# Kernel tuning notes

Measured on AMD Instinct MI355X. Metric: run time of the kernel, lower is better.

Reference implementation:

```python
import jax, jax.numpy as jnp
import numpy as np

B, T, C = 8, 512, 1024
H, E = 16, 64          # n_head, head_dim; H*E == C
L = 2048               # cached (prefix) length in the KV cache


def setup_inputs() -> dict:
    key = jax.random.key(0)
    ks = jax.random.split(key, 6)
    scale = 0.02
    return {
        "x": jax.random.normal(ks[0], (B, T, C), jnp.float32),
        "k_cache": jax.random.normal(ks[1], (B, H, L, E), jnp.float32),
        "v_cache": jax.random.normal(ks[2], (B, H, L, E), jnp.float32),
        "Wqkv": jax.random.normal(ks[3], (C, 3 * C), jnp.float32) * scale,
        "bqkv": jnp.zeros((3 * C,), jnp.float32),
        "Wproj": jax.random.normal(ks[4], (C, C), jnp.float32) * scale,
        "bproj": jnp.zeros((C,), jnp.float32),
    }


def reference(x, k_cache, v_cache, Wqkv, bqkv, Wproj, bproj):
    qkv = x @ Wqkv + bqkv
    q, k, v = jnp.split(qkv, 3, axis=-1)

    def to_heads(t):
        return t.reshape(B, T, H, E).transpose(0, 2, 1, 3)

    q, k, v = to_heads(q), to_heads(k), to_heads(v)

    # append new k,v to the cache (kv_cache.update + get)
    k_full = jnp.concatenate([k_cache, k], axis=2)  # (B,H,L+T,E)
    v_full = jnp.concatenate([v_cache, v], axis=2)

    # manual self-attention with cache-offset causal mask: row i (global pos L+i)
    # may attend to cols j <= L+i  (bias[L:L+T, :L+T])
    att = jnp.einsum("bhte,bhse->bhts", q, k_full) * (1.0 / np.sqrt(E))
    i = jnp.arange(T)[:, None] + L
    j = jnp.arange(L + T)[None, :]
    att = jnp.where(j <= i, att, -jnp.inf)
    att = jax.nn.softmax(att, axis=-1)

    y = jnp.einsum("bhts,bhse->bhte", att, v_full)
    y = y.transpose(0, 2, 1, 3).reshape(B, T, C)
    return y @ Wproj + bproj
```

## Files before the change

### kernel.cpp

```cpp
#include <hip/hip_runtime.h>
#include <hip/hip_bf16.h>

typedef unsigned short u16;
typedef unsigned int u32;

constexpr int B_ = 8, T_ = 512, C_ = 1024, H_ = 16, E_ = 64, L_ = 2048;
constexpr int S_ = L_ + T_;

typedef __bf16 bf16x8 __attribute__((ext_vector_type(8)));
typedef float f32x4 __attribute__((ext_vector_type(4)));
typedef float f32x16 __attribute__((ext_vector_type(16)));

#define QSCALE 0.18033688011112042f

__device__ inline u16 f2bf(float f) {
  u32 u = __float_as_uint(f);
  u32 r = (u + 0x7fffu + ((u >> 16) & 1u)) >> 16;
  return (u16)r;
}

__device__ inline u32 pk2(float a, float b) {
  union { __hip_bfloat162 h; u32 u; } cv;
  cv.h = __float22bfloat162_rn(float2{a, b});
  return cv.u;
}

__device__ inline void pl32swap(u32& a, u32& b) {
  asm("v_permlane32_swap_b32 %0, %1" : "+v"(a), "+v"(b));
}

__device__ inline void gload_lds16(const u16* g, u16* l) {
  __builtin_amdgcn_global_load_lds(
      (const __attribute__((address_space(1))) u32*)g,
      (__attribute__((address_space(3))) u32*)l, 16, 0, 0);
}

__global__ __launch_bounds__(256) void convert_f32_bf16(const float* __restrict__ in,
                                                        u16* __restrict__ out) {
  const int i = blockIdx.x * 256 + threadIdx.x;
  const float4 a0 = ((const float4*)in)[i * 2];
  const float4 a1 = ((const float4*)in)[i * 2 + 1];
  uint4 p;
  p.x = pk2(a0.x, a0.y);
  p.y = pk2(a0.z, a0.w);
  p.z = pk2(a1.x, a1.y);
  p.w = pk2(a1.z, a1.w);
  ((uint4*)out)[i] = p;
}

__global__ __launch_bounds__(256) void transpose_f32_bf16(const float* __restrict__ in,
                                                          u16* __restrict__ out,
                                                          int R, int Ccols) {
  __shared__ u16 tile[64][65];
  const int r0 = blockIdx.y * 64;
  const int c0 = blockIdx.x * 64;
  const int tr = threadIdx.x >> 6;
  const int tc = threadIdx.x & 63;
#pragma unroll
  for (int i = 0; i < 16; ++i)
    tile[tr + i * 4][tc] = f2bf(in[(size_t)(r0 + tr + i * 4) * Ccols + c0 + tc]);
  __syncthreads();
#pragma unroll
  for (int i = 0; i < 16; ++i)
    out[(size_t)(c0 + tr + i * 4) * R + r0 + tc] = tile[tc][tr + i * 4];
}

__global__ __launch_bounds__(256) void prep_kv(const float* __restrict__ kc,
                                               const float* __restrict__ vc,
                                               u16* __restrict__ Km,
                                               u16* __restrict__ Vtm) {
  __shared__ u16 vt[64 * 72];
  const int s0 = (blockIdx.x & 31) * 64;
  const int bh = blockIdx.x >> 5;
  const int tid = threadIdx.x;
  const int srow = tid >> 2;
  const int eq = (tid & 3) * 16;

  {
    const float* kp = kc + ((size_t)bh * L_ + s0 + srow) * E_ + eq;
    float kv[16];
    *(float4*)(kv + 0) = *(const float4*)(kp + 0);
    *(float4*)(kv + 4) = *(const float4*)(kp + 4);
    *(float4*)(kv + 8) = *(const float4*)(kp + 8);
    *(float4*)(kv + 12) = *(const float4*)(kp + 12);
    uint4 p0, p1;
    p0.x = pk2(kv[0], kv[1]);
    p0.y = pk2(kv[2], kv[3]);
    p0.z = pk2(kv[4], kv[5]);
    p0.w = pk2(kv[6], kv[7]);
    p1.x = pk2(kv[8], kv[9]);
    p1.y = pk2(kv[10], kv[11]);
    p1.z = pk2(kv[12], kv[13]);
    p1.w = pk2(kv[14], kv[15]);
    u16* kd = Km + ((size_t)bh * S_ + s0 + srow) * E_ + eq;
    *(uint4*)kd = p0;
    *(uint4*)(kd + 8) = p1;
  }
  {
    const float* vp = vc + ((size_t)bh * L_ + s0 + srow) * E_ + eq;
    float vv[16];
    *(float4*)(vv + 0) = *(const float4*)(vp + 0);
    *(float4*)(vv + 4) = *(const float4*)(vp + 4);
    *(float4*)(vv + 8) = *(const float4*)(vp + 8);
    *(float4*)(vv + 12) = *(const float4*)(vp + 12);
    uint4 p0, p1;
    p0.x = pk2(vv[0], vv[1]);
    p0.y = pk2(vv[2], vv[3]);
    p0.z = pk2(vv[4], vv[5]);
    p0.w = pk2(vv[6], vv[7]);
    p1.x = pk2(vv[8], vv[9]);
    p1.y = pk2(vv[10], vv[11]);
    p1.z = pk2(vv[12], vv[13]);
    p1.w = pk2(vv[14], vv[15]);
    *(uint4*)(vt + srow * 72 + eq) = p0;
    *(uint4*)(vt + srow * 72 + eq + 8) = p1;
  }
  __syncthreads();
  {
    const int erow = tid >> 2;
    const int sq = (tid & 3) * 16;
    u16 o[16];
#pragma unroll
    for (int j = 0; j < 16; ++j) o[j] = vt[(sq + j) * 72 + erow];
    u16* vd = Vtm + ((size_t)bh * E_ + erow) * S_ + s0 + sq;
    *(uint4*)vd = *(uint4*)(o + 0);
    *(uint4*)(vd + 8) = *(uint4*)(o + 8);
  }
}

template <int MODE>
__global__ __launch_bounds__(256) void gemm128(const u16* __restrict__ A,
                                               const u16* __restrict__ BT,
                                               const float* __restrict__ bias,
                                               u16* __restrict__ qh,
                                               u16* __restrict__ Km,
                                               u16* __restrict__ Vtm,
                                               float* __restrict__ outf,
                                               int M, int N, int K) {
  __shared__ __align__(16) u16 As[128 * 32];
  __shared__ __align__(16) u16 Bs[128 * 32];
  const int tid = threadIdx.x;
  const int lane = tid & 63;
  const int w = tid >> 6;
  const int m0 = blockIdx.y * 128;
  const int n0 = blockIdx.x * 128;
  const int wm = (w >> 1) * 64;
  const int wn = (w & 1) * 64;
  const int fm = lane & 15;
  const int fk = (lane >> 4) * 8;

  const int srow = w * 16 + (lane >> 2);
  const int scol = (lane & 3) * 8;
  const u16* Ag = A + (size_t)(m0 + srow) * K + scol;
  const u16* Bg = BT + (size_t)(n0 + srow) * K + scol;
  u16* AsU = As + w * 512;
  u16* BsU = Bs + w * 512;

  f32x4 acc[4][4];
#pragma unroll
  for (int i = 0; i < 4; ++i)
#pragma unroll
    for (int j = 0; j < 4; ++j) acc[i][j] = f32x4{0.f, 0.f, 0.f, 0.f};

  for (int k0 = 0; k0 < K; k0 += 32) {
    gload_lds16(Ag, AsU);
    gload_lds16(Ag + (size_t)64 * K, AsU + 2048);
    gload_lds16(Bg, BsU);
    gload_lds16(Bg + (size_t)64 * K, BsU + 2048);
    Ag += 32;
    Bg += 32;
    __syncthreads();
    bf16x8 af[4], bf[4];
#pragma unroll
    for (int i = 0; i < 4; ++i)
      af[i] = *(const bf16x8*)(As + (wm + i * 16 + fm) * 32 + fk);
#pragma unroll
    for (int j = 0; j < 4; ++j)
      bf[j] = *(const bf16x8*)(Bs + (wn + j * 16 + fm) * 32 + fk);
#pragma unroll
    for (int i = 0; i < 4; ++i)
#pragma unroll
      for (int j = 0; j < 4; ++j)
        acc[i][j] = __builtin_amdgcn_mfma_f32_16x16x32_bf16(af[i], bf[j], acc[i][j], 0, 0, 0);
    __syncthreads();
  }

  const int rbase = (lane >> 4) * 4;
  const int cbase = lane & 15;
#pragma unroll
  for (int i = 0; i < 4; ++i)
#pragma unroll
    for (int j = 0; j < 4; ++j) {
      const int n = n0 + wn + j * 16 + cbase;
      const float bv = bias[n];
#pragma unroll
      for (int r = 0; r < 4; ++r) {
        const int m = m0 + wm + i * 16 + rbase + r;
        const float v = acc[i][j][r] + bv;
        if (MODE == 0) {
          const int seg = n >> 10;
          const int c = n & 1023;
          const int e = c & 63;
          const int bhh = ((m >> 9) * H_) + (c >> 6);
          const int t = m & 511;
          if (seg == 0)
            qh[((size_t)bhh * T_ + t) * E_ + e] = f2bf(v * QSCALE);
          else if (seg == 1)
            Km[((size_t)bhh * S_ + L_ + t) * E_ + e] = f2bf(v);
          else
            Vtm[((size_t)bhh * E_ + e) * S_ + L_ + t] = f2bf(v);
        } else {
          outf[(size_t)m * N + n] = v;
        }
      }
    }
}

__global__ __launch_bounds__(256, 2) void attn_v4(const u16* __restrict__ qh,
                                                  const u16* __restrict__ Km,
                                                  const u16* __restrict__ Vtm,
                                                  u16* __restrict__ y2) {
  __shared__ __align__(16) u16 Ks[2][64 * 64];
  __shared__ __align__(16) u16 Vts[2][64 * 64];

  const int tid = threadIdx.x;
  const int lane = tid & 63;
  const int w = tid >> 6;
  const int bh = blockIdx.x & 127;
  const int qt = blockIdx.x >> 7;
  const int h = bh & (H_ - 1);
  const int b = bh >> 4;
  const int t0 = qt * 128;

  const int ln = lane & 31;
  const int hi = lane >> 5;
  const int swz = ln & 7;

  const u16* qbase = qh + ((size_t)bh * T_ + t0 + w * 32 + ln) * E_;
  bf16x8 qf[4];
#pragma unroll
  for (int et = 0; et < 4; ++et)
    qf[et] = *(const bf16x8*)(qbase + et * 16 + hi * 8);

  const int srow = tid >> 2;
  const int su = (tid & 3) * 2;
  const u16* kg = Km + ((size_t)bh * S_ + srow) * E_ + su * 8;
  const u16* vg = Vtm + ((size_t)bh * E_ + srow) * S_ + su * 8;
  const int st0 = srow * 64 + ((su ^ (srow & 7)) * 8);
  const int st1 = srow * 64 + (((su + 1) ^ (srow & 7)) * 8);

  f32x16 Yt[2], lacc;
#pragma unroll
  for (int i = 0; i < 16; ++i) {
    Yt[0][i] = 0.f;
    Yt[1][i] = 0.f;
    lacc[i] = 0.f;
  }

  const bf16x8 ones = {(__bf16)1.f, (__bf16)1.f, (__bf16)1.f, (__bf16)1.f,
                       (__bf16)1.f, (__bf16)1.f, (__bf16)1.f, (__bf16)1.f};

  const int qmin_w = L_ + t0 + w * 32;
  const int nchunk = (L_ + t0 + 128) >> 6;

  uint4 kr0 = *(const uint4*)(kg);
  uint4 kr1 = *(const uint4*)(kg + 8);
  uint4 vr0 = *(const uint4*)(vg);
  uint4 vr1 = *(const uint4*)(vg + 8);
  {
    u16* kd = Ks[0];
    u16* vd = Vts[0];
    *(uint4*)(kd + st0) = kr0;
    *(uint4*)(kd + st1) = kr1;
    *(uint4*)(vd + st0) = vr0;
    *(uint4*)(vd + st1) = vr1;
  }
  __syncthreads();

  for (int c = 0; c < nchunk; ++c) {
    const int sbase = c << 6;
    const u16* ks = Ks[c & 1];
    const u16* vs = Vts[c & 1];
    const bool more = (c + 1 < nchunk);

    if (more) {
      const size_t ko = (size_t)(c + 1) * 64 * E_;
      const int vo = (c + 1) * 64;
      kr0 = *(const uint4*)(kg + ko);
      kr1 = *(const uint4*)(kg + ko + 8);
      vr0 = *(const uint4*)(vg + vo);
      vr1 = *(const uint4*)(vg + vo + 8);
    }

    if (sbase <= qmin_w + 31) {
      bf16x8 pa[4];
#pragma unroll
      for (int kb = 0; kb < 2; ++kb) {
        f32x16 s;
#pragma unroll
        for (int i = 0; i < 16; ++i) s[i] = 0.f;
#pragma unroll
        for (int et = 0; et < 4; ++et) {
          const bf16x8 kf = *(const bf16x8*)(
              ks + (kb * 32 + ln) * 64 + (((et * 2 + hi) ^ swz) * 8));
          s = __builtin_amdgcn_mfma_f32_32x32x16_bf16(kf, qf[et], s, 0, 0, 0);
        }

        if (sbase + 63 > qmin_w) {
          const int qpos = qmin_w + ln;
          const int kb0 = sbase + kb * 32 + hi * 4;
#pragma unroll
          for (int r = 0; r < 16; ++r) {
            const int keypos = kb0 + (r & 3) + 8 * (r >> 2);
            if (keypos > qpos) s[r] = -1e30f;
          }
        }

#pragma unroll
        for (int r = 0; r < 16; ++r) s[r] = exp2f(s[r]);

#pragma unroll
        for (int t = 0; t < 2; ++t) {
          u32 x0 = pk2(s[8 * t + 0], s[8 * t + 1]);
          u32 y0 = pk2(s[8 * t + 4], s[8 * t + 5]);
          u32 x1 = pk2(s[8 * t + 2], s[8 * t + 3]);
          u32 y1 = pk2(s[8 * t + 6], s[8 * t + 7]);
          pl32swap(x0, y0);
          pl32swap(x1, y1);
          union { u32 u[4]; bf16x8 v; } pu;
          pu.u[0] = x0;
          pu.u[1] = x1;
          pu.u[2] = y0;
          pu.u[3] = y1;
          pa[kb * 2 + t] = pu.v;
        }
      }

#pragma unroll
      for (int t = 0; t < 4; ++t)
        lacc = __builtin_amdgcn_mfma_f32_32x32x16_bf16(ones, pa[t], lacc, 0, 0, 0);

#pragma unroll
      for (int eb = 0; eb < 2; ++eb)
#pragma unroll
        for (int t = 0; t < 4; ++t) {
          const bf16x8 vf = *(const bf16x8*)(
              vs + (eb * 32 + ln) * 64 + (((t * 2 + hi) ^ swz) * 8));
          Yt[eb] = __builtin_amdgcn_mfma_f32_32x32x16_bf16(vf, pa[t], Yt[eb], 0, 0, 0);
        }
    }

    if (more) {
      u16* kd = Ks[(c + 1) & 1];
      u16* vd = Vts[(c + 1) & 1];
      *(uint4*)(kd + st0) = kr0;
      *(uint4*)(kd + st1) = kr1;
      *(uint4*)(vd + st0) = vr0;
      *(uint4*)(vd + st1) = vr1;
    }
    __syncthreads();
  }

  const float rl = 1.f / lacc[0];
  const int t_out = t0 + w * 32 + ln;
  u16* yp = y2 + ((size_t)b * T_ + t_out) * C_ + h * E_ + hi * 4;
#pragma unroll
  for (int eb = 0; eb < 2; ++eb)
#pragma unroll
    for (int g = 0; g < 4; ++g) {
      uint2 st;
      st.x = pk2(Yt[eb][4 * g + 0] * rl, Yt[eb][4 * g + 1] * rl);
      st.y = pk2(Yt[eb][4 * g + 2] * rl, Yt[eb][4 * g + 3] * rl);
      *(uint2*)(yp + eb * 32 + g * 8) = st;
    }
}

extern "C" void kernel_launch(void* const* d_in, const int* in_sizes, int n_in,
                              void* d_out, int out_size, void* d_ws, size_t ws_size,
                              hipStream_t stream) {
  const float* x = (const float*)d_in[0];
  const float* kc = (const float*)d_in[1];
  const float* vc = (const float*)d_in[2];
  const float* Wqkv = (const float*)d_in[3];
  const float* bqkv = (const float*)d_in[4];
  const float* Wproj = (const float*)d_in[5];
  const float* bproj = (const float*)d_in[6];
  float* out = (float*)d_out;

  u16* qh = (u16*)d_ws;
  u16* y2 = qh + 4194304;
  u16* xb = y2 + 4194304;
  u16* WqT = xb + 4194304;
  u16* WpT = WqT + 3145728;
  u16* Km = WpT + 1048576;
  u16* Vtm = Km + 20971520;

  convert_f32_bf16<<<dim3(2048), 256, 0, stream>>>(x, xb);
  transpose_f32_bf16<<<dim3(48, 16), 256, 0, stream>>>(Wqkv, WqT, 1024, 3072);
  transpose_f32_bf16<<<dim3(16, 16), 256, 0, stream>>>(Wproj, WpT, 1024, 1024);
  prep_kv<<<dim3(128 * 32), 256, 0, stream>>>(kc, vc, Km, Vtm);

  gemm128<0><<<dim3(24, 32), 256, 0, stream>>>(xb, WqT, bqkv, qh, Km, Vtm, nullptr,
                                               4096, 3072, 1024);

  attn_v4<<<dim3(512), 256, 0, stream>>>(qh, Km, Vtm, y2);

  gemm128<1><<<dim3(8, 32), 256, 0, stream>>>(y2, WpT, bproj, nullptr, nullptr,
                                              nullptr, out, 4096, 1024, 1024);
}
```

Baseline: 343.6 us.

## Load K/V fragments directly from global in attention; stage new V via transpose kernel

The attention kernel stops staging K and V tiles through double-buffered shared memory with block barriers. Each wave now loads its K and V MFMA fragments straight from global memory and software-pipelines the next K chunk in registers. Each wave also computes its own causal chunk count and applies the mask only on its last chunk. The QKV GEMM now writes new V rows coalesced into a scratch buffer (y2), and a separate vtrans kernel transposes them into the V-transposed cache, avoiding strided scatter stores. The cost is extra global and L2 traffic with no cross-wave reuse of K/V through LDS, one more kernel launch, and higher register pressure.

Result: slower. 408.1 us (+18.8%).

```diff
diff --git a/kernel.cpp b/kernel.cpp
--- a/kernel.cpp
+++ b/kernel.cpp
@@ -128,13 +128,35 @@
   }
 }
 
+__global__ __launch_bounds__(256) void vtrans(const u16* __restrict__ vh,
+                                              u16* __restrict__ Vtm) {
+  __shared__ u16 vt[64 * 72];
+  const int t0 = (blockIdx.x & 7) * 64;
+  const int bh = blockIdx.x >> 3;
+  const int tid = threadIdx.x;
+  const int srow = tid >> 2;
+  const int eq = (tid & 3) * 16;
+  const u16* vp = vh + ((size_t)bh * T_ + t0 + srow) * E_ + eq;
+  *(uint4*)(vt + srow * 72 + eq) = *(const uint4*)vp;
+  *(uint4*)(vt + srow * 72 + eq + 8) = *(const uint4*)(vp + 8);
+  __syncthreads();
+  const int erow = tid >> 2;
+  const int sq = (tid & 3) * 16;
+  u16 o[16];
+#pragma unroll
+  for (int j = 0; j < 16; ++j) o[j] = vt[(sq + j) * 72 + erow];
+  u16* vd = Vtm + ((size_t)bh * E_ + erow) * S_ + L_ + t0 + sq;
+  *(uint4*)vd = *(uint4*)(o + 0);
+  *(uint4*)(vd + 8) = *(uint4*)(o + 8);
+}
+
 template <int MODE>
 __global__ __launch_bounds__(256) void gemm128(const u16* __restrict__ A,
                                                const u16* __restrict__ BT,
                                                const float* __restrict__ bias,
                                                u16* __restrict__ qh,
                                                u16* __restrict__ Km,
-                                               u16* __restrict__ Vtm,
+                                               u16* __restrict__ vout,
                                                float* __restrict__ outf,
                                                int M, int N, int K) {
   __shared__ __align__(16) u16 As[128 * 32];
@@ -208,7 +230,7 @@
           else if (seg == 1)
             Km[((size_t)bhh * S_ + L_ + t) * E_ + e] = f2bf(v);
           else
-            Vtm[((size_t)bhh * E_ + e) * S_ + L_ + t] = f2bf(v);
+            vout[((size_t)bhh * T_ + t) * E_ + e] = f2bf(v);
         } else {
           outf[(size_t)m * N + n] = v;
         }
@@ -216,13 +238,58 @@
     }
 }
 
-__global__ __launch_bounds__(256, 2) void attn_v4(const u16* __restrict__ qh,
+#define ATTN_CHUNK(KF, KN, cc)                                                   \
+  {                                                                              \
+    const int sbase = (cc) << 6;                                                 \
+    const int cpf = ((cc) + 1 < nck) ? (cc) + 1 : nck - 1;                       \
+    bf16x8 vf[2][4];                                                             \
+    _Pragma("unroll") for (int eb = 0; eb < 2; ++eb)                             \
+      _Pragma("unroll") for (int t = 0; t < 4; ++t)                              \
+        vf[eb][t] = *(const bf16x8*)(Vl + (size_t)eb * 32 * S_ + (cc) * 64 + t * 16); \
+    bf16x8 pa[4];                                                                \
+    _Pragma("unroll") for (int kb = 0; kb < 2; ++kb) {                           \
+      f32x16 s;                                                                  \
+      _Pragma("unroll") for (int i = 0; i < 16; ++i) s[i] = 0.f;                 \
+      _Pragma("unroll") for (int et = 0; et < 4; ++et)                           \
+        s = __builtin_amdgcn_mfma_f32_32x32x16_bf16(KF[kb][et], qf[et], s, 0, 0, 0); \
+      if ((cc) == nck - 1) {                                                     \
+        const int mb = sbase + kb * 32 + hi * 4;                                 \
+        _Pragma("unroll") for (int r = 0; r < 16; ++r) {                         \
+          const int keypos = mb + (r & 3) + 8 * (r >> 2);                        \
+          if (keypos > qpos) s[r] = -1e30f;                                      \
+        }                                                                        \
+      }                                                                          \
+      _Pragma("unroll") for (int r = 0; r < 16; ++r) s[r] = exp2f(s[r]);         \
+      _Pragma("unroll") for (int t = 0; t < 2; ++t) {                            \
+        u32 x0 = pk2(s[8 * t + 0], s[8 * t + 1]);                                \
+        u32 y0 = pk2(s[8 * t + 4], s[8 * t + 5]);                                \
+        u32 x1 = pk2(s[8 * t + 2], s[8 * t + 3]);                                \
+        u32 y1 = pk2(s[8 * t + 6], s[8 * t + 7]);                                \
+        pl32swap(x0, y0);                                                        \
+        pl32swap(x1, y1);                                                        \
+        union { u32 u[4]; bf16x8 v; } pu;                                        \
+        pu.u[0] = x0;                                                            \
+        pu.u[1] = x1;                                                            \
+        pu.u[2] = y0;                                                            \
+        pu.u[3] = y1;                                                            \
+        pa[kb * 2 + t] = pu.v;                                                   \
+      }                                                                          \
+    }                                                                            \
+    _Pragma("unroll") for (int kb = 0; kb < 2; ++kb)                             \
+      _Pragma("unroll") for (int et = 0; et < 4; ++et)                           \
+        KN[kb][et] = *(const bf16x8*)(Kl + ((size_t)cpf * 64 + kb * 32) * E_ + et * 16); \
+    _Pragma("unroll") for (int t = 0; t < 4; ++t)                                \
+      lacc = __builtin_amdgcn_mfma_f32_32x32x16_bf16(ones, pa[t], lacc, 0, 0, 0); \
+    _Pragma("unroll") for (int t = 0; t < 4; ++t)                                \
+      Yt[0] = __builtin_amdgcn_mfma_f32_32x32x16_bf16(vf[0][t], pa[t], Yt[0], 0, 0, 0); \
+    _Pragma("unroll") for (int t = 0; t < 4; ++t)                                \
+      Yt[1] = __builtin_amdgcn_mfma_f32_32x32x16_bf16(vf[1][t], pa[t], Yt[1], 0, 0, 0); \
+  }
+
+__global__ __launch_bounds__(256, 2) void attn_v5(const u16* __restrict__ qh,
                                                   const u16* __restrict__ Km,
                                                   const u16* __restrict__ Vtm,
                                                   u16* __restrict__ y2) {
-  __shared__ __align__(16) u16 Ks[2][64 * 64];
-  __shared__ __align__(16) u16 Vts[2][64 * 64];
-
   const int tid = threadIdx.x;
   const int lane = tid & 63;
   const int w = tid >> 6;
@@ -234,7 +301,6 @@
 
   const int ln = lane & 31;
   const int hi = lane >> 5;
-  const int swz = ln & 7;
 
   const u16* qbase = qh + ((size_t)bh * T_ + t0 + w * 32 + ln) * E_;
   bf16x8 qf[4];
@@ -242,12 +308,12 @@
   for (int et = 0; et < 4; ++et)
     qf[et] = *(const bf16x8*)(qbase + et * 16 + hi * 8);
 
-  const int srow = tid >> 2;
-  const int su = (tid & 3) * 2;
-  const u16* kg = Km + ((size_t)bh * S_ + srow) * E_ + su * 8;
-  const u16* vg = Vtm + ((size_t)bh * E_ + srow) * S_ + su * 8;
-  const int st0 = srow * 64 + ((su ^ (srow & 7)) * 8);
-  const int st1 = srow * 64 + (((su + 1) ^ (srow & 7)) * 8);
+  const int qmin = L_ + t0 + w * 32;
+  const int qpos = qmin + ln;
+  const int nck = (qmin + 32 + 63) >> 6;
+
+  const u16* Kl = Km + ((size_t)bh * S_ + ln) * E_ + hi * 8;
+  const u16* Vl = Vtm + ((size_t)bh * E_ + ln) * S_ + hi * 8;
 
   f32x16 Yt[2], lacc;
 #pragma unroll
@@ -260,105 +326,19 @@
   const bf16x8 ones = {(__bf16)1.f, (__bf16)1.f, (__bf16)1.f, (__bf16)1.f,
                        (__bf16)1.f, (__bf16)1.f, (__bf16)1.f, (__bf16)1.f};
 
-  const int qmin_w = L_ + t0 + w * 32;
-  const int nchunk = (L_ + t0 + 128) >> 6;
-
-  uint4 kr0 = *(const uint4*)(kg);
-  uint4 kr1 = *(const uint4*)(kg + 8);
-  uint4 vr0 = *(const uint4*)(vg);
-  uint4 vr1 = *(const uint4*)(vg + 8);
-  {
-    u16* kd = Ks[0];
-    u16* vd = Vts[0];
-    *(uint4*)(kd + st0) = kr0;
-    *(uint4*)(kd + st1) = kr1;
-    *(uint4*)(vd + st0) = vr0;
-    *(uint4*)(vd + st1) = vr1;
-  }
-  __syncthreads();
-
-  for (int c = 0; c < nchunk; ++c) {
-    const int sbase = c << 6;
-    const u16* ks = Ks[c & 1];
-    const u16* vs = Vts[c & 1];
-    const bool more = (c + 1 < nchunk);
-
-    if (more) {
-      const size_t ko = (size_t)(c + 1) * 64 * E_;
-      const int vo = (c + 1) * 64;
-      kr0 = *(const uint4*)(kg + ko);
-      kr1 = *(const uint4*)(kg + ko + 8);
-      vr0 = *(const uint4*)(vg + vo);
-      vr1 = *(const uint4*)(vg + vo + 8);
-    }
-
-    if (sbase <= qmin_w + 31) {
-      bf16x8 pa[4];
-#pragma unroll
-      for (int kb = 0; kb < 2; ++kb) {
-        f32x16 s;
-#pragma unroll
-        for (int i = 0; i < 16; ++i) s[i] = 0.f;
-#pragma unroll
-        for (int et = 0; et < 4; ++et) {
-          const bf16x8 kf = *(const bf16x8*)(
-              ks + (kb * 32 + ln) * 64 + (((et * 2 + hi) ^ swz) * 8));
-          s = __builtin_amdgcn_mfma_f32_32x32x16_bf16(kf, qf[et], s, 0, 0, 0);
-        }
-
-        if (sbase + 63 > qmin_w) {
-          const int qpos = qmin_w + ln;
-          const int kb0 = sbase + kb * 32 + hi * 4;
-#pragma unroll
-          for (int r = 0; r < 16; ++r) {
-            const int keypos = kb0 + (r & 3) + 8 * (r >> 2);
-            if (keypos > qpos) s[r] = -1e30f;
-          }
-        }
-
-#pragma unroll
-        for (int r = 0; r < 16; ++r) s[r] = exp2f(s[r]);
-
-#pragma unroll
-        for (int t = 0; t < 2; ++t) {
-          u32 x0 = pk2(s[8 * t + 0], s[8 * t + 1]);
-          u32 y0 = pk2(s[8 * t + 4], s[8 * t + 5]);
-          u32 x1 = pk2(s[8 * t + 2], s[8 * t + 3]);
-          u32 y1 = pk2(s[8 * t + 6], s[8 * t + 7]);
-          pl32swap(x0, y0);
-          pl32swap(x1, y1);
-          union { u32 u[4]; bf16x8 v; } pu;
-          pu.u[0] = x0;
-          pu.u[1] = x1;
-          pu.u[2] = y0;
-          pu.u[3] = y1;
-          pa[kb * 2 + t] = pu.v;
-        }
-      }
-
-#pragma unroll
-      for (int t = 0; t < 4; ++t)
-        lacc = __builtin_amdgcn_mfma_f32_32x32x16_bf16(ones, pa[t], lacc, 0, 0, 0);
-
-#pragma unroll
-      for (int eb = 0; eb < 2; ++eb)
-#pragma unroll
-        for (int t = 0; t < 4; ++t) {
-          const bf16x8 vf = *(const bf16x8*)(
-              vs + (eb * 32 + ln) * 64 + (((t * 2 + hi) ^ swz) * 8));
-          Yt[eb] = __builtin_amdgcn_mfma_f32_32x32x16_bf16(vf, pa[t], Yt[eb], 0, 0, 0);
-        }
-    }
-
-    if (more) {
-      u16* kd = Ks[(c + 1) & 1];
-      u16* vd = Vts[(c + 1) & 1];
-      *(uint4*)(kd + st0) = kr0;
-      *(uint4*)(kd + st1) = kr1;
-      *(uint4*)(vd + st0) = vr0;
-      *(uint4*)(vd + st1) = vr1;
-    }
-    __syncthreads();
+  bf16x8 kA[2][4], kB[2][4];
+#pragma unroll
+  for (int kb = 0; kb < 2; ++kb)
+#pragma unroll
+    for (int et = 0; et < 4; ++et)
+      kA[kb][et] = *(const bf16x8*)(Kl + (size_t)(kb * 32) * E_ + et * 16);
+
+  int c = 0;
+  while (true) {
+    ATTN_CHUNK(kA, kB, c);
+    if (++c >= nck) break;
+    ATTN_CHUNK(kB, kA, c);
+    if (++c >= nck) break;
   }
 
   const float rl = 1.f / lacc[0];
@@ -400,10 +380,11 @@
   transpose_f32_bf16<<<dim3(16, 16), 256, 0, stream>>>(Wproj, WpT, 1024, 1024);
   prep_kv<<<dim3(128 * 32), 256, 0, stream>>>(kc, vc, Km, Vtm);
 
-  gemm128<0><<<dim3(24, 32), 256, 0, stream>>>(xb, WqT, bqkv, qh, Km, Vtm, nullptr,
+  gemm128<0><<<dim3(24, 32), 256, 0, stream>>>(xb, WqT, bqkv, qh, Km, y2, nullptr,
                                                4096, 3072, 1024);
-
-  attn_v4<<<dim3(512), 256, 0, stream>>>(qh, Km, Vtm, y2);
+  vtrans<<<dim3(128 * 8), 256, 0, stream>>>(y2, Vtm);
+
+  attn_v5<<<dim3(512), 256, 0, stream>>>(qh, Km, Vtm, y2);
 
   gemm128<1><<<dim3(8, 32), 256, 0, stream>>>(y2, WpT, bproj, nullptr, nullptr,
                                               nullptr, out, 4096, 1024, 1024);
```

## Split KV chunks across two wave groups in attention and coalesce V transpose

Applied to the files above, without the earlier changes.

The attention kernel now runs 512 threads per block. Two groups of four waves each process alternate 64-key chunks for the same 128 queries, and their partial outputs and row sums are merged through shared memory at the end. The QKV GEMM now writes new V values row-major into a scratch buffer, and a separate vtrans kernel transposes them into the V-transposed cache, replacing the scattered strided stores. The goal is more parallelism and latency hiding per block and better store coalescing. The cost is an extra kernel launch, a larger shared-memory footprint, and a reduction step at the end.

Result: slower. 355.4 us (+3.4%).

```diff
diff --git a/kernel.cpp b/kernel.cpp
--- a/kernel.cpp
+++ b/kernel.cpp
@@ -128,13 +128,35 @@
   }
 }
 
+__global__ __launch_bounds__(256) void vtrans(const u16* __restrict__ vh,
+                                              u16* __restrict__ Vtm) {
+  __shared__ u16 vt[64 * 72];
+  const int t0 = (blockIdx.x & 7) * 64;
+  const int bh = blockIdx.x >> 3;
+  const int tid = threadIdx.x;
+  const int srow = tid >> 2;
+  const int eq = (tid & 3) * 16;
+  const u16* vp = vh + ((size_t)bh * T_ + t0 + srow) * E_ + eq;
+  *(uint4*)(vt + srow * 72 + eq) = *(const uint4*)vp;
+  *(uint4*)(vt + srow * 72 + eq + 8) = *(const uint4*)(vp + 8);
+  __syncthreads();
+  const int erow = tid >> 2;
+  const int sq = (tid & 3) * 16;
+  u16 o[16];
+#pragma unroll
+  for (int j = 0; j < 16; ++j) o[j] = vt[(sq + j) * 72 + erow];
+  u16* vd = Vtm + ((size_t)bh * E_ + erow) * S_ + L_ + t0 + sq;
+  *(uint4*)vd = *(uint4*)(o + 0);
+  *(uint4*)(vd + 8) = *(uint4*)(o + 8);
+}
+
 template <int MODE>
 __global__ __launch_bounds__(256) void gemm128(const u16* __restrict__ A,
                                                const u16* __restrict__ BT,
                                                const float* __restrict__ bias,
                                                u16* __restrict__ qh,
                                                u16* __restrict__ Km,
-                                               u16* __restrict__ Vtm,
+                                               u16* __restrict__ vout,
                                                float* __restrict__ outf,
                                                int M, int N, int K) {
   __shared__ __align__(16) u16 As[128 * 32];
@@ -208,7 +230,7 @@
           else if (seg == 1)
             Km[((size_t)bhh * S_ + L_ + t) * E_ + e] = f2bf(v);
           else
-            Vtm[((size_t)bhh * E_ + e) * S_ + L_ + t] = f2bf(v);
+            vout[((size_t)bhh * T_ + t) * E_ + e] = f2bf(v);
         } else {
           outf[(size_t)m * N + n] = v;
         }
@@ -216,16 +238,19 @@
     }
 }
 
-__global__ __launch_bounds__(256, 2) void attn_v4(const u16* __restrict__ qh,
+__global__ __launch_bounds__(512, 4) void attn_v6(const u16* __restrict__ qh,
                                                   const u16* __restrict__ Km,
                                                   const u16* __restrict__ Vtm,
                                                   u16* __restrict__ y2) {
-  __shared__ __align__(16) u16 Ks[2][64 * 64];
-  __shared__ __align__(16) u16 Vts[2][64 * 64];
+  __shared__ __align__(16) u16 smem[32768];
+  u16* KsB = smem;
+  u16* VtsB = smem + 16384;
 
   const int tid = threadIdx.x;
   const int lane = tid & 63;
   const int w = tid >> 6;
+  const int wq = w & 3;
+  const int par = w >> 2;
   const int bh = blockIdx.x & 127;
   const int qt = blockIdx.x >> 7;
   const int h = bh & (H_ - 1);
@@ -236,40 +261,47 @@
   const int hi = lane >> 5;
   const int swz = ln & 7;
 
-  const u16* qbase = qh + ((size_t)bh * T_ + t0 + w * 32 + ln) * E_;
+  const u16* qbase = qh + ((size_t)bh * T_ + t0 + wq * 32 + ln) * E_;
   bf16x8 qf[4];
 #pragma unroll
   for (int et = 0; et < 4; ++et)
     qf[et] = *(const bf16x8*)(qbase + et * 16 + hi * 8);
 
-  const int srow = tid >> 2;
-  const int su = (tid & 3) * 2;
+  const int tq = tid & 255;
+  const int sp = tid >> 8;
+  const int srow = tq >> 2;
+  const int su = (tq & 3) * 2;
   const u16* kg = Km + ((size_t)bh * S_ + srow) * E_ + su * 8;
   const u16* vg = Vtm + ((size_t)bh * E_ + srow) * S_ + su * 8;
   const int st0 = srow * 64 + ((su ^ (srow & 7)) * 8);
   const int st1 = srow * 64 + (((su + 1) ^ (srow & 7)) * 8);
 
-  f32x16 Yt[2], lacc;
+  f32x16 Yt[2], lacc, zero16;
 #pragma unroll
   for (int i = 0; i < 16; ++i) {
     Yt[0][i] = 0.f;
     Yt[1][i] = 0.f;
     lacc[i] = 0.f;
+    zero16[i] = 0.f;
   }
 
   const bf16x8 ones = {(__bf16)1.f, (__bf16)1.f, (__bf16)1.f, (__bf16)1.f,
                        (__bf16)1.f, (__bf16)1.f, (__bf16)1.f, (__bf16)1.f};
 
-  const int qmin_w = L_ + t0 + w * 32;
+  const int qmin_w = L_ + t0 + wq * 32;
+  const int qpos = qmin_w + ln;
   const int nchunk = (L_ + t0 + 128) >> 6;
-
-  uint4 kr0 = *(const uint4*)(kg);
-  uint4 kr1 = *(const uint4*)(kg + 8);
-  uint4 vr0 = *(const uint4*)(vg);
-  uint4 vr1 = *(const uint4*)(vg + 8);
+  const int npair = nchunk >> 1;
+
   {
-    u16* kd = Ks[0];
-    u16* vd = Vts[0];
+    const size_t ko = (size_t)sp * 64 * E_;
+    const int vo = sp * 64;
+    uint4 kr0 = *(const uint4*)(kg + ko);
+    uint4 kr1 = *(const uint4*)(kg + ko + 8);
+    uint4 vr0 = *(const uint4*)(vg + vo);
+    uint4 vr1 = *(const uint4*)(vg + vo + 8);
+    u16* kd = KsB + sp * 4096;
+    u16* vd = VtsB + sp * 4096;
     *(uint4*)(kd + st0) = kr0;
     *(uint4*)(kd + st1) = kr1;
     *(uint4*)(vd + st0) = vr0;
@@ -277,41 +309,42 @@
   }
   __syncthreads();
 
-  for (int c = 0; c < nchunk; ++c) {
-    const int sbase = c << 6;
-    const u16* ks = Ks[c & 1];
-    const u16* vs = Vts[c & 1];
-    const bool more = (c + 1 < nchunk);
-
+  for (int i = 0; i < npair; ++i) {
+    const int hlf = i & 1;
+    const int cs = 2 * (i + 1) + sp;
+    const bool more = cs < nchunk;
+    uint4 kr0, kr1, vr0, vr1;
     if (more) {
-      const size_t ko = (size_t)(c + 1) * 64 * E_;
-      const int vo = (c + 1) * 64;
+      const size_t ko = (size_t)cs * 64 * E_;
+      const int vo = cs * 64;
       kr0 = *(const uint4*)(kg + ko);
       kr1 = *(const uint4*)(kg + ko + 8);
       vr0 = *(const uint4*)(vg + vo);
       vr1 = *(const uint4*)(vg + vo + 8);
     }
 
+    const int cmy = 2 * i + par;
+    const int sbase = cmy << 6;
     if (sbase <= qmin_w + 31) {
+      const u16* ks = KsB + (hlf * 2 + par) * 4096;
+      const u16* vs = VtsB + (hlf * 2 + par) * 4096;
       bf16x8 pa[4];
 #pragma unroll
       for (int kb = 0; kb < 2; ++kb) {
         f32x16 s;
-#pragma unroll
-        for (int i = 0; i < 16; ++i) s[i] = 0.f;
 #pragma unroll
         for (int et = 0; et < 4; ++et) {
           const bf16x8 kf = *(const bf16x8*)(
               ks + (kb * 32 + ln) * 64 + (((et * 2 + hi) ^ swz) * 8));
-          s = __builtin_amdgcn_mfma_f32_32x32x16_bf16(kf, qf[et], s, 0, 0, 0);
+          s = __builtin_amdgcn_mfma_f32_32x32x16_bf16(kf, qf[et],
+                                                      et == 0 ? zero16 : s, 0, 0, 0);
         }
 
         if (sbase + 63 > qmin_w) {
-          const int qpos = qmin_w + ln;
-          const int kb0 = sbase + kb * 32 + hi * 4;
+          const int mb = sbase + kb * 32 + hi * 4;
 #pragma unroll
           for (int r = 0; r < 16; ++r) {
-            const int keypos = kb0 + (r & 3) + 8 * (r >> 2);
+            const int keypos = mb + (r & 3) + 8 * (r >> 2);
             if (keypos > qpos) s[r] = -1e30f;
           }
         }
@@ -351,8 +384,8 @@
     }
 
     if (more) {
-      u16* kd = Ks[(c + 1) & 1];
-      u16* vd = Vts[(c + 1) & 1];
+      u16* kd = KsB + ((hlf ^ 1) * 2 + sp) * 4096;
+      u16* vd = VtsB + ((hlf ^ 1) * 2 + sp) * 4096;
       *(uint4*)(kd + st0) = kr0;
       *(uint4*)(kd + st1) = kr1;
       *(uint4*)(vd + st0) = vr0;
@@ -361,18 +394,36 @@
     __syncthreads();
   }
 
-  const float rl = 1.f / lacc[0];
-  const int t_out = t0 + w * 32 + ln;
-  u16* yp = y2 + ((size_t)b * T_ + t_out) * C_ + h * E_ + hi * 4;
-#pragma unroll
-  for (int eb = 0; eb < 2; ++eb)
-#pragma unroll
-    for (int g = 0; g < 4; ++g) {
-      uint2 st;
-      st.x = pk2(Yt[eb][4 * g + 0] * rl, Yt[eb][4 * g + 1] * rl);
-      st.y = pk2(Yt[eb][4 * g + 2] * rl, Yt[eb][4 * g + 3] * rl);
-      *(uint2*)(yp + eb * 32 + g * 8) = st;
-    }
+  float* red = (float*)smem;
+  if (par == 1) {
+    float* rp = red + ((size_t)(wq * 64 + lane)) * 34;
+#pragma unroll
+    for (int i = 0; i < 16; ++i) rp[i] = Yt[0][i];
+#pragma unroll
+    for (int i = 0; i < 16; ++i) rp[16 + i] = Yt[1][i];
+    rp[32] = lacc[0];
+  }
+  __syncthreads();
+  if (par == 0) {
+    const float* rp = red + ((size_t)(wq * 64 + lane)) * 34;
+#pragma unroll
+    for (int i = 0; i < 16; ++i) Yt[0][i] += rp[i];
+#pragma unroll
+    for (int i = 0; i < 16; ++i) Yt[1][i] += rp[16 + i];
+    const float rl = 1.f / (lacc[0] + rp[32]);
+
+    const int t_out = t0 + wq * 32 + ln;
+    u16* yp = y2 + ((size_t)b * T_ + t_out) * C_ + h * E_ + hi * 4;
+#pragma unroll
+    for (int eb = 0; eb < 2; ++eb)
+#pragma unroll
+      for (int g = 0; g < 4; ++g) {
+        uint2 st;
+        st.x = pk2(Yt[eb][4 * g + 0] * rl, Yt[eb][4 * g + 1] * rl);
+        st.y = pk2(Yt[eb][4 * g + 2] * rl, Yt[eb][4 * g + 3] * rl);
+        *(uint2*)(yp + eb * 32 + g * 8) = st;
+      }
+  }
 }
 
 extern "C" void kernel_launch(void* const* d_in, const int* in_sizes, int n_in,
@@ -400,10 +451,11 @@
   transpose_f32_bf16<<<dim3(16, 16), 256, 0, stream>>>(Wproj, WpT, 1024, 1024);
   prep_kv<<<dim3(128 * 32), 256, 0, stream>>>(kc, vc, Km, Vtm);
 
-  gemm128<0><<<dim3(24, 32), 256, 0, stream>>>(xb, WqT, bqkv, qh, Km, Vtm, nullptr,
+  gemm128<0><<<dim3(24, 32), 256, 0, stream>>>(xb, WqT, bqkv, qh, Km, y2, nullptr,
                                                4096, 3072, 1024);
-
-  attn_v4<<<dim3(512), 256, 0, stream>>>(qh, Km, Vtm, y2);
+  vtrans<<<dim3(128 * 8), 256, 0, stream>>>(y2, Vtm);
+
+  attn_v6<<<dim3(512), 512, 0, stream>>>(qh, Km, Vtm, y2);
 
   gemm128<1><<<dim3(8, 32), 256, 0, stream>>>(y2, WpT, bproj, nullptr, nullptr,
                                               nullptr, out, 4096, 1024, 1024);
```

## Pre-swizzle K/V in global memory and stream tiles via direct global-to-LDS loads

Applied to the files above, without the earlier changes.

The attention kernel stops staging K/V tiles through registers. It now issues global_load_lds transfers straight into a triple-buffered LDS ring, prefetching two chunks ahead and synchronising with explicit vmcnt waits and barriers. Because the direct-to-LDS path cannot apply the XOR swizzle, the producers (prep_kv and the QKV GEMM epilogue) now write K and V^T into global memory already swizzled. pk2 also switches to an inline v_cvt_pk_bf16_f32 instruction, and the first MFMA of each score tile now starts from a zero accumulator. This trades a larger LDS footprint and tighter coupling of layouts across kernels for less register pressure and more overlap of memory traffic with compute.

Measured after the change: 335.7 us. 2.3% less time.

```diff
diff --git a/kernel.cpp b/kernel.cpp
--- a/kernel.cpp
+++ b/kernel.cpp
@@ -12,6 +12,7 @@
 typedef float f32x16 __attribute__((ext_vector_type(16)));
 
 #define QSCALE 0.18033688011112042f
+
 
 __device__ inline u16 f2bf(float f) {
   u32 u = __float_as_uint(f);
@@ -20,9 +21,9 @@
 }
 
 __device__ inline u32 pk2(float a, float b) {
-  union { __hip_bfloat162 h; u32 u; } cv;
-  cv.h = __float22bfloat162_rn(float2{a, b});
-  return cv.u;
+  u32 r;
+  asm("v_cvt_pk_bf16_f32 %0, %1, %2" : "=v"(r) : "v"(a), "v"(b));
+  return r;
 }
 
 __device__ inline void pl32swap(u32& a, u32& b) {
@@ -92,9 +93,10 @@
     p1.y = pk2(kv[10], kv[11]);
     p1.z = pk2(kv[12], kv[13]);
     p1.w = pk2(kv[14], kv[15]);
-    u16* kd = Km + ((size_t)bh * S_ + s0 + srow) * E_ + eq;
-    *(uint4*)kd = p0;
-    *(uint4*)(kd + 8) = p1;
+    const int sx = (srow & 7) << 3;
+    u16* kd = Km + ((size_t)bh * S_ + s0 + srow) * E_;
+    *(uint4*)(kd + (eq ^ sx)) = p0;
+    *(uint4*)(kd + ((eq + 8) ^ sx)) = p1;
   }
   {
     const float* vp = vc + ((size_t)bh * L_ + s0 + srow) * E_ + eq;
@@ -122,9 +124,10 @@
     u16 o[16];
 #pragma unroll
     for (int j = 0; j < 16; ++j) o[j] = vt[(sq + j) * 72 + erow];
-    u16* vd = Vtm + ((size_t)bh * E_ + erow) * S_ + s0 + sq;
-    *(uint4*)vd = *(uint4*)(o + 0);
-    *(uint4*)(vd + 8) = *(uint4*)(o + 8);
+    const int ex = (erow & 7) << 3;
+    u16* vd = Vtm + ((size_t)bh * E_ + erow) * S_ + s0;
+    *(uint4*)(vd + (sq ^ ex)) = *(uint4*)(o + 0);
+    *(uint4*)(vd + ((sq + 8) ^ ex)) = *(uint4*)(o + 8);
   }
 }
 
@@ -206,9 +209,9 @@
           if (seg == 0)
             qh[((size_t)bhh * T_ + t) * E_ + e] = f2bf(v * QSCALE);
           else if (seg == 1)
-            Km[((size_t)bhh * S_ + L_ + t) * E_ + e] = f2bf(v);
+            Km[((size_t)bhh * S_ + L_ + t) * E_ + (e ^ ((t & 7) << 3))] = f2bf(v);
           else
-            Vtm[((size_t)bhh * E_ + e) * S_ + L_ + t] = f2bf(v);
+            Vtm[((size_t)bhh * E_ + e) * S_ + ((L_ + t) ^ ((e & 7) << 3))] = f2bf(v);
         } else {
           outf[(size_t)m * N + n] = v;
         }
@@ -216,12 +219,12 @@
     }
 }
 
-__global__ __launch_bounds__(256, 2) void attn_v4(const u16* __restrict__ qh,
+__global__ __launch_bounds__(256, 2) void attn_v8(const u16* __restrict__ qh,
                                                   const u16* __restrict__ Km,
                                                   const u16* __restrict__ Vtm,
                                                   u16* __restrict__ y2) {
-  __shared__ __align__(16) u16 Ks[2][64 * 64];
-  __shared__ __align__(16) u16 Vts[2][64 * 64];
+  __shared__ __align__(16) u16 Ksf[3 * 4096];
+  __shared__ __align__(16) u16 Vtsf[3 * 4096];
 
   const int tid = threadIdx.x;
   const int lane = tid & 63;
@@ -242,82 +245,74 @@
   for (int et = 0; et < 4; ++et)
     qf[et] = *(const bf16x8*)(qbase + et * 16 + hi * 8);
 
-  const int srow = tid >> 2;
-  const int su = (tid & 3) * 2;
-  const u16* kg = Km + ((size_t)bh * S_ + srow) * E_ + su * 8;
-  const u16* vg = Vtm + ((size_t)bh * E_ + srow) * S_ + su * 8;
-  const int st0 = srow * 64 + ((su ^ (srow & 7)) * 8);
-  const int st1 = srow * 64 + (((su + 1) ^ (srow & 7)) * 8);
-
-  f32x16 Yt[2], lacc;
+  const int l8 = lane >> 3;
+  const int u8 = lane & 7;
+  const u16* kgl = Km + ((size_t)bh * S_ + w * 16 + l8) * E_ + u8 * 8;
+  const u16* vgl = Vtm + ((size_t)bh * E_ + w * 16 + l8) * S_ + u8 * 8;
+  const int kdst = w * 1024;
+
+#define STAGE(cc, bi)                                                       \
+  do {                                                                      \
+    gload_lds16(kgl + (size_t)(cc) * 64 * E_, Ksf + (bi) * 4096 + kdst);    \
+    gload_lds16(kgl + ((size_t)(cc) * 64 + 8) * E_,                         \
+                Ksf + (bi) * 4096 + kdst + 512);                            \
+    gload_lds16(vgl + (cc) * 64, Vtsf + (bi) * 4096 + kdst);                \
+    gload_lds16(vgl + (size_t)8 * S_ + (cc) * 64,                           \
+                Vtsf + (bi) * 4096 + kdst + 512);                           \
+  } while (0)
+
+  f32x16 Yt[2], lacc, zero16;
 #pragma unroll
   for (int i = 0; i < 16; ++i) {
     Yt[0][i] = 0.f;
     Yt[1][i] = 0.f;
     lacc[i] = 0.f;
+    zero16[i] = 0.f;
   }
 
   const bf16x8 ones = {(__bf16)1.f, (__bf16)1.f, (__bf16)1.f, (__bf16)1.f,
                        (__bf16)1.f, (__bf16)1.f, (__bf16)1.f, (__bf16)1.f};
 
   const int qmin_w = L_ + t0 + w * 32;
+  const int qpos = qmin_w + ln;
   const int nchunk = (L_ + t0 + 128) >> 6;
 
-  uint4 kr0 = *(const uint4*)(kg);
-  uint4 kr1 = *(const uint4*)(kg + 8);
-  uint4 vr0 = *(const uint4*)(vg);
-  uint4 vr1 = *(const uint4*)(vg + 8);
-  {
-    u16* kd = Ks[0];
-    u16* vd = Vts[0];
-    *(uint4*)(kd + st0) = kr0;
-    *(uint4*)(kd + st1) = kr1;
-    *(uint4*)(vd + st0) = vr0;
-    *(uint4*)(vd + st1) = vr1;
-  }
-  __syncthreads();
-
+  STAGE(0, 0);
+  STAGE(1, 1);
+  asm volatile("s_waitcnt vmcnt(4)" ::: "memory");
+  __builtin_amdgcn_s_barrier();
+
+  int i0 = 0, i1 = 1, i2 = 2;
   for (int c = 0; c < nchunk; ++c) {
-    const int sbase = c << 6;
-    const u16* ks = Ks[c & 1];
-    const u16* vs = Vts[c & 1];
-    const bool more = (c + 1 < nchunk);
-
-    if (more) {
-      const size_t ko = (size_t)(c + 1) * 64 * E_;
-      const int vo = (c + 1) * 64;
-      kr0 = *(const uint4*)(kg + ko);
-      kr1 = *(const uint4*)(kg + ko + 8);
-      vr0 = *(const uint4*)(vg + vo);
-      vr1 = *(const uint4*)(vg + vo + 8);
-    }
-
-    if (sbase <= qmin_w + 31) {
+    if (c + 2 < nchunk) STAGE(c + 2, i2);
+
+    if ((c << 6) <= qmin_w + 31) {
+      const int sbase = c << 6;
+      const u16* ks = Ksf + i0 * 4096;
+      const u16* vs = Vtsf + i0 * 4096;
       bf16x8 pa[4];
 #pragma unroll
       for (int kb = 0; kb < 2; ++kb) {
         f32x16 s;
-#pragma unroll
-        for (int i = 0; i < 16; ++i) s[i] = 0.f;
 #pragma unroll
         for (int et = 0; et < 4; ++et) {
           const bf16x8 kf = *(const bf16x8*)(
               ks + (kb * 32 + ln) * 64 + (((et * 2 + hi) ^ swz) * 8));
-          s = __builtin_amdgcn_mfma_f32_32x32x16_bf16(kf, qf[et], s, 0, 0, 0);
+          s = __builtin_amdgcn_mfma_f32_32x32x16_bf16(kf, qf[et],
+                                                      et == 0 ? zero16 : s, 0, 0, 0);
         }
 
         if (sbase + 63 > qmin_w) {
-          const int qpos = qmin_w + ln;
-          const int kb0 = sbase + kb * 32 + hi * 4;
-#pragma unroll
-          for (int r = 0; r < 16; ++r) {
-            const int keypos = kb0 + (r & 3) + 8 * (r >> 2);
-            if (keypos > qpos) s[r] = -1e30f;
+          const int mb = sbase + kb * 32 + hi * 4;
+#pragma unroll
+          for (int rr = 0; rr < 16; ++rr) {
+            const int keypos = mb + (rr & 3) + 8 * (rr >> 2);
+            if (keypos > qpos) s[rr] = -1e30f;
           }
         }
 
 #pragma unroll
-        for (int r = 0; r < 16; ++r) s[r] = exp2f(s[r]);
+        for (int rr = 0; rr < 16; ++rr) s[rr] = exp2f(s[rr]);
 
 #pragma unroll
         for (int t = 0; t < 2; ++t) {
@@ -350,16 +345,18 @@
         }
     }
 
-    if (more) {
-      u16* kd = Ks[(c + 1) & 1];
-      u16* vd = Vts[(c + 1) & 1];
-      *(uint4*)(kd + st0) = kr0;
-      *(uint4*)(kd + st1) = kr1;
-      *(uint4*)(vd + st0) = vr0;
-      *(uint4*)(vd + st1) = vr1;
-    }
-    __syncthreads();
-  }
+    if (c + 2 < nchunk)
+      asm volatile("s_waitcnt vmcnt(4)" ::: "memory");
+    else if (c + 1 < nchunk)
+      asm volatile("s_waitcnt vmcnt(0)" ::: "memory");
+    if (c + 1 < nchunk) __builtin_amdgcn_s_barrier();
+
+    const int tmp = i0;
+    i0 = i1;
+    i1 = i2;
+    i2 = tmp;
+  }
+#undef STAGE
 
   const float rl = 1.f / lacc[0];
   const int t_out = t0 + w * 32 + ln;
@@ -403,7 +400,7 @@
   gemm128<0><<<dim3(24, 32), 256, 0, stream>>>(xb, WqT, bqkv, qh, Km, Vtm, nullptr,
                                                4096, 3072, 1024);
 
-  attn_v4<<<dim3(512), 256, 0, stream>>>(qh, Km, Vtm, y2);
+  attn_v8<<<dim3(512), 256, 0, stream>>>(qh, Km, Vtm, y2);
 
   gemm128<1><<<dim3(8, 32), 256, 0, stream>>>(y2, WpT, bproj, nullptr, nullptr,
                                               nullptr, out, 4096, 1024, 1024);
```
